# Kernel optimization log

Measured on AMD Instinct MI355X. Metric: run time of the kernel, lower is better.

The kernel has to match this reference:

```python
import jax, jax.numpy as jnp
import numpy as np

B, NC, NT = 16, 2048, 2048
IN_DIM, H_DIM, OUT_DIM = 128, 256, 256


def _mlp(x, w1, b1, w2, b2, w3, b3):
    # MLP(input_dim, [h, h], output_dim): Linear-ReLU-Linear-ReLU-Linear
    h = jax.nn.relu(x @ w1 + b1)
    h = jax.nn.relu(h @ w2 + b2)
    return h @ w3 + b3


def setup_inputs() -> dict:
    key = jax.random.key(0)
    ks = jax.random.split(key, 16)

    def lin(k, fan_in, fan_out):
        s = 1.0 / np.sqrt(fan_in)
        kw, kb = jax.random.split(k)
        w = jax.random.uniform(kw, (fan_in, fan_out), jnp.float32, -s, s)
        b = jax.random.uniform(kb, (fan_out,), jnp.float32, -s, s)
        return w, b

    qw1, qb1 = lin(ks[0], IN_DIM, H_DIM)
    qw2, qb2 = lin(ks[1], H_DIM, H_DIM)
    qw3, qb3 = lin(ks[2], H_DIM, OUT_DIM)
    kw1, kb1 = lin(ks[3], IN_DIM, H_DIM)
    kw2, kb2 = lin(ks[4], H_DIM, H_DIM)
    kw3, kb3 = lin(ks[5], H_DIM, OUT_DIM)

    return {
        "x_context": jax.random.normal(ks[6], (B, NC, IN_DIM), jnp.float32),
        "x_target": jax.random.normal(ks[7], (B, NT, IN_DIM), jnp.float32),
        "r_i": jax.random.normal(ks[8], (B, NC, OUT_DIM), jnp.float32),
        "qw1": qw1, "qb1": qb1, "qw2": qw2, "qb2": qb2, "qw3": qw3, "qb3": qb3,
        "kw1": kw1, "kb1": kb1, "kw2": kw2, "kb2": kb2, "kw3": kw3, "kb3": kb3,
    }


def reference(x_context, x_target, r_i,
              qw1, qb1, qw2, qb2, qw3, qb3,
              kw1, kb1, kw2, kb2, kw3, kb3):
    q = _mlp(x_target, qw1, qb1, qw2, qb2, qw3, qb3)   # [B, NT, D]
    k = _mlp(x_context, kw1, kb1, kw2, kb2, kw3, kb3)  # [B, NC, D]
    scale = jnp.sqrt(jnp.asarray(k.shape[-1], dtype=jnp.float32))
    w = jnp.einsum('btd,bcd->btc', q, k) / scale       # [B, NT, NC]
    # Faithful to torch.softmax(w, dim=1): normalize over the TARGET axis.
    w = jax.nn.softmax(w, axis=1)
    return jnp.einsum('btc,bcd->btd', w, r_i)          # [B, NT, OUT_DIM]
```

## Files before the change

kernel.cpp:

```cpp
#include <hip/hip_runtime.h>

#define BB 16
#define NT 2048
#define NC 2048
#define DIM 256
#define INDIM 128

typedef unsigned short u16;
typedef __bf16 bfx8 __attribute__((ext_vector_type(8)));
typedef __bf16 bfx8a __attribute__((ext_vector_type(8), aligned(8)));
typedef float f32x4 __attribute__((ext_vector_type(4)));

__device__ __forceinline__ u16 f2bf(float f) {
    union { float f; unsigned u; } v; v.f = f;
    return (u16)((v.u + 0x7FFFu + ((v.u >> 16) & 1u)) >> 16);
}

#define MFMA16(a, b, c) __builtin_amdgcn_mfma_f32_16x16x32_bf16((a), (b), (c), 0, 0, 0)


__global__ void cvt_w_kernel(const float* __restrict__ w, u16* __restrict__ wt, int K) {
    int idx = blockIdx.x * 256 + threadIdx.x;
    if (idx >= K * 256) return;
    int n = idx / K, k = idx - n * K;
    wt[idx] = f2bf(w[k * 256 + n]);
}

__global__ void cvt_rt_kernel(const float* __restrict__ r, u16* __restrict__ rt) {
    __shared__ u16 tile[32][33];
    int b = blockIdx.z;
    int c0 = blockIdx.x * 32, d0 = blockIdx.y * 32;
    int tx = threadIdx.x, ty = threadIdx.y;
    const float* rb = r + (size_t)b * NC * DIM;
#pragma unroll
    for (int i = 0; i < 4; i++) {
        int c = c0 + ty + i * 8;
        tile[ty + i * 8][tx] = f2bf(rb[(size_t)c * DIM + d0 + tx]);
    }
    __syncthreads();
    u16* rtb = rt + (size_t)b * DIM * NC;
#pragma unroll
    for (int i = 0; i < 4; i++) {
        int d = d0 + ty + i * 8;
        rtb[(size_t)d * NC + c0 + tx] = tile[tx][ty + i * 8];
    }
}


template <int K, bool RELU, bool CVTIN>
__global__ __launch_bounds__(256) void mlp_gemm(const void* __restrict__ Aq, const void* __restrict__ Ak,
                                                const u16* __restrict__ Wq, const u16* __restrict__ Wk,
                                                const float* __restrict__ bq, const float* __restrict__ bk,
                                                u16* __restrict__ Cq, u16* __restrict__ Ck) {
    constexpr int ROWB = K * 2;
    constexpr int NCH = K / 16;
    __shared__ __align__(16) u16 at[128 * K];

    int tid = threadIdx.x, lane = tid & 63, w = tid >> 6;
    int lr = lane & 15, lg = lane >> 4;
    int m0 = blockIdx.x * 128;
    bool isq = (blockIdx.y == 0);
    const u16* Wt = isq ? Wq : Wk;
    const float* bias = isq ? bq : bk;
    u16* C = isq ? Cq : Ck;

    if (CVTIN) {
        const float* A = (const float*)(isq ? Aq : Ak) + (size_t)m0 * K;
#pragma unroll
        for (int j = 0; j < NCH; j++) {
            int bo = tid * (NCH * 16) + j * 16;
            int row = bo >> 8;
            int ir = bo & (ROWB - 1);
            const float* src = A + (size_t)row * K + (ir >> 1);
            float4 f0 = *reinterpret_cast<const float4*>(src);
            float4 f1 = *reinterpret_cast<const float4*>(src + 4);
            union { u16 u[8]; uint4 v; } pk;
            {
                __bf16 h;
                h = (__bf16)f0.x; pk.u[0] = *(u16*)&h;
                h = (__bf16)f0.y; pk.u[1] = *(u16*)&h;
                h = (__bf16)f0.z; pk.u[2] = *(u16*)&h;
                h = (__bf16)f0.w; pk.u[3] = *(u16*)&h;
                h = (__bf16)f1.x; pk.u[4] = *(u16*)&h;
                h = (__bf16)f1.y; pk.u[5] = *(u16*)&h;
                h = (__bf16)f1.z; pk.u[6] = *(u16*)&h;
                h = (__bf16)f1.w; pk.u[7] = *(u16*)&h;
            }
            int dst = row * ROWB + (ir ^ ((row & 7) << 4));
            *reinterpret_cast<uint4*>((char*)at + dst) = pk.v;
        }
    } else {
        const char* A = (const char*)((const u16*)(isq ? Aq : Ak) + (size_t)m0 * K);
#pragma unroll
        for (int j = 0; j < NCH; j++) {
            int bo = j * 4096 + tid * 16;
            int row = bo >> 9;
            int ir = bo & (ROWB - 1);
            int sir = ir ^ ((row & 7) << 4);
            __builtin_amdgcn_global_load_lds(
                (const __attribute__((address_space(1))) void*)(A + (size_t)row * ROWB + sir),
                (__attribute__((address_space(3))) void*)((char*)at + bo),
                16, 0, 0);
        }
    }
    __syncthreads();

    int n0 = w * 64;
    f32x4 acc[8][4] = {};
#pragma unroll
    for (int ks = 0; ks < K / 32; ks++) {
        bfx8 b[4];
#pragma unroll
        for (int nt = 0; nt < 4; nt++)
            b[nt] = *reinterpret_cast<const bfx8*>(Wt + (size_t)(n0 + nt * 16 + lr) * K + ks * 32 + lg * 8);
#pragma unroll
        for (int mt = 0; mt < 8; mt++) {
            int row = mt * 16 + lr;
            int ir = (ks * 64 + lg * 16) ^ ((lr & 7) << 4);
            bfx8 a = *reinterpret_cast<const bfx8*>((const char*)at + row * ROWB + ir);
#pragma unroll
            for (int nt = 0; nt < 4; nt++)
                acc[mt][nt] = MFMA16(a, b[nt], acc[mt][nt]);
        }
    }

#pragma unroll
    for (int nt = 0; nt < 4; nt++) {
        int col = n0 + nt * 16 + lr;
        float bv = bias[col];
#pragma unroll
        for (int mt = 0; mt < 8; mt++) {
            int rowb = m0 + mt * 16 + lg * 4;
#pragma unroll
            for (int r = 0; r < 4; r++) {
                float v = acc[mt][nt][r] + bv;
                if (RELU) v = fmaxf(v, 0.0f);
                C[(size_t)(rowb + r) * 256 + col] = f2bf(v);
            }
        }
    }
}


__global__ __launch_bounds__(256) void stats_kernel(const u16* __restrict__ q,
                                                    const u16* __restrict__ k,
                                                    float2* __restrict__ gso) {
    int flat = blockIdx.x;
    int sw = (flat & 7) * 64 + (flat >> 3);
    int b = sw >> 5;
    int c0 = (sw & 31) * 64;
    int tid = threadIdx.x, lane = tid & 63, w = tid >> 6;
    int lr = lane & 15, lg = lane >> 4;
    const u16* qb = q + (size_t)b * NT * DIM;
    const u16* kb = k + (size_t)b * NC * DIM;
    const float scale = 1.0f / 16.0f;

    bfx8 kf[4][8];
#pragma unroll
    for (int j = 0; j < 4; j++)
#pragma unroll
        for (int ks = 0; ks < 8; ks++)
            kf[j][ks] = *reinterpret_cast<const bfx8*>(kb + (size_t)(c0 + j * 16 + lr) * DIM + ks * 32 + lg * 8);

    float m_run[4], l_run[4];
#pragma unroll
    for (int j = 0; j < 4; j++) { m_run[j] = -1e30f; l_run[j] = 0.0f; }

    for (int ts = 0; ts < NT / 64; ts++) {
        int t0 = ts * 64 + w * 16;
        f32x4 acc[4] = {};
#pragma unroll
        for (int ks = 0; ks < 8; ks++) {
            bfx8 a = *reinterpret_cast<const bfx8*>(qb + (size_t)(t0 + lr) * DIM + ks * 32 + lg * 8);
#pragma unroll
            for (int j = 0; j < 4; j++)
                acc[j] = MFMA16(a, kf[j][ks], acc[j]);
        }
#pragma unroll
        for (int j = 0; j < 4; j++) {
            float s0 = acc[j][0] * scale, s1 = acc[j][1] * scale;
            float s2 = acc[j][2] * scale, s3 = acc[j][3] * scale;
            float mx = fmaxf(fmaxf(s0, s1), fmaxf(s2, s3));
            mx = fmaxf(mx, __shfl_xor(mx, 16));
            mx = fmaxf(mx, __shfl_xor(mx, 32));
            float m_new = fmaxf(m_run[j], mx);
            float p = __expf(s0 - m_new) + __expf(s1 - m_new) + __expf(s2 - m_new) + __expf(s3 - m_new);
            p += __shfl_xor(p, 16);
            p += __shfl_xor(p, 32);
            l_run[j] = l_run[j] * __expf(m_run[j] - m_new) + p;
            m_run[j] = m_new;
        }
    }

    __shared__ float sm[4][64], sl[4][64];
    if (lg == 0) {
#pragma unroll
        for (int j = 0; j < 4; j++) {
            sm[w][j * 16 + lr] = m_run[j];
            sl[w][j * 16 + lr] = l_run[j];
        }
    }
    __syncthreads();
    if (tid < 64) {
        float mf = sm[0][tid];
#pragma unroll
        for (int ww = 1; ww < 4; ww++) mf = fmaxf(mf, sm[ww][tid]);
        float lf = 0.0f;
#pragma unroll
        for (int ww = 0; ww < 4; ww++) lf += sl[ww][tid] * __expf(sm[ww][tid] - mf);
        gso[(size_t)b * NC + c0 + tid] = make_float2(mf * 1.44269504f, 1.0f / lf);
    }
}


__global__ __launch_bounds__(256, 2) void attn_kernel(const u16* __restrict__ q,
                                                      const u16* __restrict__ k,
                                                      const u16* __restrict__ rt,
                                                      const float2* __restrict__ gsg_,
                                                      float* __restrict__ out) {
    int flat = blockIdx.x;
    int sw = (flat & 7) * 64 + (flat >> 3);
    int b = sw >> 5;
    int t0 = (sw & 31) * 64;
    int tid = threadIdx.x, lane = tid & 63, w = tid >> 6;
    int lr = lane & 15, lg = lane >> 4;
    const u16* qb = q + (size_t)b * NT * DIM;
    const u16* kb = k + (size_t)b * NC * DIM;
    const u16* rtb = rt + (size_t)b * DIM * NC;

    __shared__ float2 gs[NC];
    __shared__ __align__(16) u16 kt[2][32 * 256];
    __shared__ u16 pl[64][36];

    {
        const float2* gsg = gsg_ + (size_t)b * NC;
        for (int i = tid; i < NC; i += 256) gs[i] = gsg[i];
    }
    __syncthreads();

#define STAGE(nb, cc) do {                                                          \
    const u16* ksrc_ = kb + (size_t)(cc) * DIM;                                     \
    _Pragma("unroll")                                                               \
    for (int i_ = 0; i_ < 4; i_++) {                                                \
        int off_ = ((w * 4 + i_) << 10) + (lane << 4);                              \
        int row_ = off_ >> 9;                                                       \
        int ss_  = ((off_ >> 4) & 31) ^ (row_ & 7);                                 \
        const u16* g_ = ksrc_ + row_ * DIM + ss_ * 8;                               \
        __builtin_amdgcn_global_load_lds(                                           \
            (const __attribute__((address_space(1))) void*)g_,                      \
            (__attribute__((address_space(3))) void*)(&kt[nb][(w * 4 + i_) << 9]),  \
            16, 0, 0);                                                              \
    }                                                                               \
} while (0)

    STAGE(0, 0);
    __builtin_amdgcn_sched_barrier(0);
    bfx8 rb_c[4], rb_n[4];
#pragma unroll
    for (int nt = 0; nt < 4; nt++)
        rb_c[nt] = *reinterpret_cast<const bfx8*>(rtb + (size_t)(w * 64 + nt * 16 + lr) * NC + lg * 8);
    bfx8 aq[8];
#pragma unroll
    for (int ks = 0; ks < 8; ks++)
        aq[ks] = *reinterpret_cast<const bfx8*>(qb + (size_t)(t0 + w * 16 + lr) * DIM + ks * 32 + lg * 8);
    __builtin_amdgcn_sched_barrier(0);
    asm volatile("s_waitcnt vmcnt(12)");
    __builtin_amdgcn_s_barrier();
    __builtin_amdgcn_sched_barrier(0);

    const float A = 1.44269504f / 16.0f;
    const int key = lr & 7;
    f32x4 acc[4][4] = {};
    int cur = 0;

    for (int c0 = 0; c0 < NC; c0 += 32) {
        const bool last = (c0 + 32 >= NC);
        if (!last) STAGE(cur ^ 1, c0 + 32);
        __builtin_amdgcn_sched_barrier(0);
        if (!last) {
#pragma unroll
            for (int nt = 0; nt < 4; nt++)
                rb_n[nt] = *reinterpret_cast<const bfx8*>(rtb + (size_t)(w * 64 + nt * 16 + lr) * NC + (c0 + 32) + lg * 8);
        }

        f32x4 s[2] = {};
        {
            const char* kc = (const char*)&kt[cur][0];
#pragma unroll
            for (int ks = 0; ks < 8; ks++) {
                int slot = (ks << 2) | lg;
                bfx8 k0 = *reinterpret_cast<const bfx8*>(kc + (lr << 9) + (((slot ^ key)) << 4));
                bfx8 k1 = *reinterpret_cast<const bfx8*>(kc + ((16 + lr) << 9) + (((slot ^ key)) << 4));
                s[0] = MFMA16(aq[ks], k0, s[0]);
                s[1] = MFMA16(aq[ks], k1, s[1]);
            }
        }
#pragma unroll
        for (int j = 0; j < 2; j++) {
            float2 g = gs[c0 + j * 16 + lr];
#pragma unroll
            for (int r = 0; r < 4; r++) {
                float p = exp2f(fmaf(s[j][r], A, -g.x)) * g.y;
                __bf16 h = (__bf16)p;
                pl[w * 16 + lg * 4 + r][j * 16 + lr] = *(u16*)&h;
            }
        }
        __builtin_amdgcn_sched_barrier(0);
        asm volatile("s_waitcnt lgkmcnt(0)");
        __builtin_amdgcn_s_barrier();
        __builtin_amdgcn_sched_barrier(0);

#pragma unroll
        for (int mt = 0; mt < 4; mt++) {
            bfx8a pa = *reinterpret_cast<const bfx8a*>((const char*)pl + (mt * 16 + lr) * 72 + lg * 16);
#pragma unroll
            for (int nt = 0; nt < 4; nt++)
                acc[mt][nt] = MFMA16((bfx8)pa, rb_c[nt], acc[mt][nt]);
        }

        __builtin_amdgcn_sched_barrier(0);
        asm volatile("s_waitcnt vmcnt(4) lgkmcnt(0)");
        __builtin_amdgcn_s_barrier();
        __builtin_amdgcn_sched_barrier(0);

#pragma unroll
        for (int nt = 0; nt < 4; nt++) rb_c[nt] = rb_n[nt];
        cur ^= 1;
    }
#undef STAGE

    float* ob = out + (size_t)b * NT * DIM;
#pragma unroll
    for (int nt = 0; nt < 4; nt++) {
        int col = w * 64 + nt * 16 + lr;
#pragma unroll
        for (int mt = 0; mt < 4; mt++) {
            int rowb = t0 + mt * 16 + lg * 4;
#pragma unroll
            for (int r = 0; r < 4; r++)
                ob[(size_t)(rowb + r) * DIM + col] = acc[mt][nt][r];
        }
    }
}


extern "C" void kernel_launch(void* const* d_in, const int* in_sizes, int n_in,
                              void* d_out, int out_size, void* d_ws, size_t ws_size,
                              hipStream_t stream) {
    const float* xc  = (const float*)d_in[0];
    const float* xt  = (const float*)d_in[1];
    const float* ri  = (const float*)d_in[2];
    const float* qw1 = (const float*)d_in[3];  const float* qb1 = (const float*)d_in[4];
    const float* qw2 = (const float*)d_in[5];  const float* qb2 = (const float*)d_in[6];
    const float* qw3 = (const float*)d_in[7];  const float* qb3 = (const float*)d_in[8];
    const float* kw1 = (const float*)d_in[9];  const float* kb1 = (const float*)d_in[10];
    const float* kw2 = (const float*)d_in[11]; const float* kb2 = (const float*)d_in[12];
    const float* kw3 = (const float*)d_in[13]; const float* kb3 = (const float*)d_in[14];

    if (ws_size < ((size_t)66 << 20)) return;

    char* ws = (char*)d_ws;
    u16* h1q = (u16*)(ws);
    u16* h1k = (u16*)(ws + ((size_t)16 << 20));
    u16* q   = h1q;
    u16* kk  = h1k;
    u16* h2q = (u16*)(ws + ((size_t)32 << 20));
    u16* h2k = (u16*)(ws + ((size_t)48 << 20));
    u16* rt  = h2q;
    float2* gsb = (float2*)(ws + ((size_t)64 << 20));
    u16* wbuf = (u16*)(ws + ((size_t)64 << 20) + (512 << 10));
    u16* qw1t = wbuf;
    u16* qw2t = qw1t + 32768;
    u16* qw3t = qw2t + 65536;
    u16* kw1t = qw3t + 65536;
    u16* kw2t = kw1t + 32768;
    u16* kw3t = kw2t + 65536;

    cvt_w_kernel<<<dim3(128), 256, 0, stream>>>(qw1, qw1t, 128);
    cvt_w_kernel<<<dim3(256), 256, 0, stream>>>(qw2, qw2t, 256);
    cvt_w_kernel<<<dim3(256), 256, 0, stream>>>(qw3, qw3t, 256);
    cvt_w_kernel<<<dim3(128), 256, 0, stream>>>(kw1, kw1t, 128);
    cvt_w_kernel<<<dim3(256), 256, 0, stream>>>(kw2, kw2t, 256);
    cvt_w_kernel<<<dim3(256), 256, 0, stream>>>(kw3, kw3t, 256);

    mlp_gemm<128, true,  true ><<<dim3(256, 2), 256, 0, stream>>>(xt, xc, qw1t, kw1t, qb1, kb1, h1q, h1k);
    mlp_gemm<256, true,  false><<<dim3(256, 2), 256, 0, stream>>>(h1q, h1k, qw2t, kw2t, qb2, kb2, h2q, h2k);
    mlp_gemm<256, false, false><<<dim3(256, 2), 256, 0, stream>>>(h2q, h2k, qw3t, kw3t, qb3, kb3, q, kk);

    cvt_rt_kernel<<<dim3(64, 8, BB), dim3(32, 8), 0, stream>>>(ri, rt);

    stats_kernel<<<dim3(512), 256, 0, stream>>>(q, kk, gsb);

    attn_kernel<<<dim3(512), 256, 0, stream>>>(q, kk, rt, gsb, (float*)d_out);
}
```

Baseline: 286.4 us.

## Split attention block across 8 waves, defer stats shuffles, merge weight casts

The attention kernel now runs 512 threads per block. Each wave computes one 16x16 score tile and a 32x64 slice of the output instead of 64x64, and softmax stats are streamed from global memory rather than staged in shared memory. The stats kernel drops the per-step cross-lane max/sum shuffles in favour of per-lane online stats that are merged once at the end, using exp2 with a prescaled constant. The six weight-conversion launches are fused into one. Together these aim for more waves in flight to hide latency, fewer shuffles, and less launch overhead. The trade-off is more barrier participants per block and register pressure under the new launch bounds.

```diff
diff --git a/kernel.cpp b/kernel.cpp
--- a/kernel.cpp
+++ b/kernel.cpp
@@ -19,11 +19,22 @@
 #define MFMA16(a, b, c) __builtin_amdgcn_mfma_f32_16x16x32_bf16((a), (b), (c), 0, 0, 0)
 
 
-__global__ void cvt_w_kernel(const float* __restrict__ w, u16* __restrict__ wt, int K) {
-    int idx = blockIdx.x * 256 + threadIdx.x;
-    if (idx >= K * 256) return;
+__global__ void cvt_w_all(const float* __restrict__ w0, const float* __restrict__ w1,
+                          const float* __restrict__ w2, const float* __restrict__ w3,
+                          const float* __restrict__ w4, const float* __restrict__ w5,
+                          u16* __restrict__ o0, u16* __restrict__ o1, u16* __restrict__ o2,
+                          u16* __restrict__ o3, u16* __restrict__ o4, u16* __restrict__ o5) {
+    int bx = blockIdx.x;
+    const float* src; u16* dst; int K, base;
+    if (bx < 128)       { src = w0; dst = o0; K = 128; base = 0; }
+    else if (bx < 384)  { src = w1; dst = o1; K = 256; base = 128; }
+    else if (bx < 640)  { src = w2; dst = o2; K = 256; base = 384; }
+    else if (bx < 768)  { src = w3; dst = o3; K = 128; base = 640; }
+    else if (bx < 1024) { src = w4; dst = o4; K = 256; base = 768; }
+    else                { src = w5; dst = o5; K = 256; base = 1024; }
+    int idx = (bx - base) * 256 + threadIdx.x;
     int n = idx / K, k = idx - n * K;
-    wt[idx] = f2bf(w[k * 256 + n]);
+    dst[idx] = f2bf(src[k * 256 + n]);
 }
 
 __global__ void cvt_rt_kernel(const float* __restrict__ r, u16* __restrict__ rt) {
@@ -153,7 +164,7 @@
     int lr = lane & 15, lg = lane >> 4;
     const u16* qb = q + (size_t)b * NT * DIM;
     const u16* kb = k + (size_t)b * NC * DIM;
-    const float scale = 1.0f / 16.0f;
+    const float A2 = 1.44269504f / 16.0f;
 
     bfx8 kf[4][8];
 #pragma unroll
@@ -178,18 +189,29 @@
         }
 #pragma unroll
         for (int j = 0; j < 4; j++) {
-            float s0 = acc[j][0] * scale, s1 = acc[j][1] * scale;
-            float s2 = acc[j][2] * scale, s3 = acc[j][3] * scale;
-            float mx = fmaxf(fmaxf(s0, s1), fmaxf(s2, s3));
-            mx = fmaxf(mx, __shfl_xor(mx, 16));
-            mx = fmaxf(mx, __shfl_xor(mx, 32));
-            float m_new = fmaxf(m_run[j], mx);
-            float p = __expf(s0 - m_new) + __expf(s1 - m_new) + __expf(s2 - m_new) + __expf(s3 - m_new);
-            p += __shfl_xor(p, 16);
-            p += __shfl_xor(p, 32);
-            l_run[j] = l_run[j] * __expf(m_run[j] - m_new) + p;
-            m_run[j] = m_new;
-        }
+            f32x4 a = acc[j];
+            float mx = fmaxf(fmaxf(a[0], a[1]), fmaxf(a[2], a[3]));
+            float mn = fmaxf(m_run[j], mx);
+            float t = mn * A2;
+            float sum = exp2f(fmaf(a[0], A2, -t)) + exp2f(fmaf(a[1], A2, -t)) +
+                        exp2f(fmaf(a[2], A2, -t)) + exp2f(fmaf(a[3], A2, -t));
+            l_run[j] = l_run[j] * exp2f(fmaf(m_run[j], A2, -t)) + sum;
+            m_run[j] = mn;
+        }
+    }
+
+#pragma unroll
+    for (int j = 0; j < 4; j++) {
+        float m = m_run[j], l = l_run[j];
+#pragma unroll
+        for (int d = 16; d < 64; d <<= 1) {
+            float mo = __shfl_xor(m, d);
+            float lo = __shfl_xor(l, d);
+            float mn = fmaxf(m, mo);
+            l = l * exp2f((m - mn) * A2) + lo * exp2f((mo - mn) * A2);
+            m = mn;
+        }
+        m_run[j] = m; l_run[j] = l;
     }
 
     __shared__ float sm[4][64], sl[4][64];
@@ -207,13 +229,13 @@
         for (int ww = 1; ww < 4; ww++) mf = fmaxf(mf, sm[ww][tid]);
         float lf = 0.0f;
 #pragma unroll
-        for (int ww = 0; ww < 4; ww++) lf += sl[ww][tid] * __expf(sm[ww][tid] - mf);
-        gso[(size_t)b * NC + c0 + tid] = make_float2(mf * 1.44269504f, 1.0f / lf);
-    }
-}
-
-
-__global__ __launch_bounds__(256, 2) void attn_kernel(const u16* __restrict__ q,
+        for (int ww = 0; ww < 4; ww++) lf += sl[ww][tid] * exp2f((sm[ww][tid] - mf) * A2);
+        gso[(size_t)b * NC + c0 + tid] = make_float2(mf * A2, 1.0f / lf);
+    }
+}
+
+
+__global__ __launch_bounds__(512, 4) void attn_kernel(const u16* __restrict__ q,
                                                       const u16* __restrict__ k,
                                                       const u16* __restrict__ rt,
                                                       const float2* __restrict__ gsg_,
@@ -224,53 +246,51 @@
     int t0 = (sw & 31) * 64;
     int tid = threadIdx.x, lane = tid & 63, w = tid >> 6;
     int lr = lane & 15, lg = lane >> 4;
+    int sr = w & 3, sc = w >> 2;
+    int pr = w & 1, pc = w >> 1;
     const u16* qb = q + (size_t)b * NT * DIM;
     const u16* kb = k + (size_t)b * NC * DIM;
     const u16* rtb = rt + (size_t)b * DIM * NC;
-
-    __shared__ float2 gs[NC];
+    const float2* gsg = gsg_ + (size_t)b * NC;
+
     __shared__ __align__(16) u16 kt[2][32 * 256];
     __shared__ u16 pl[64][36];
-
-    {
-        const float2* gsg = gsg_ + (size_t)b * NC;
-        for (int i = tid; i < NC; i += 256) gs[i] = gsg[i];
-    }
-    __syncthreads();
 
 #define STAGE(nb, cc) do {                                                          \
     const u16* ksrc_ = kb + (size_t)(cc) * DIM;                                     \
     _Pragma("unroll")                                                               \
-    for (int i_ = 0; i_ < 4; i_++) {                                                \
-        int off_ = ((w * 4 + i_) << 10) + (lane << 4);                              \
+    for (int i_ = 0; i_ < 2; i_++) {                                                \
+        int off_ = ((w * 2 + i_) << 10) + (lane << 4);                              \
         int row_ = off_ >> 9;                                                       \
         int ss_  = ((off_ >> 4) & 31) ^ (row_ & 7);                                 \
         const u16* g_ = ksrc_ + row_ * DIM + ss_ * 8;                               \
         __builtin_amdgcn_global_load_lds(                                           \
             (const __attribute__((address_space(1))) void*)g_,                      \
-            (__attribute__((address_space(3))) void*)(&kt[nb][(w * 4 + i_) << 9]),  \
+            (__attribute__((address_space(3))) void*)(&kt[nb][(w * 2 + i_) << 9]),  \
             16, 0, 0);                                                              \
     }                                                                               \
 } while (0)
 
     STAGE(0, 0);
     __builtin_amdgcn_sched_barrier(0);
+    float2 gs_c, gs_n;
+    gs_c = gsg[sc * 16 + lr];
     bfx8 rb_c[4], rb_n[4];
 #pragma unroll
     for (int nt = 0; nt < 4; nt++)
-        rb_c[nt] = *reinterpret_cast<const bfx8*>(rtb + (size_t)(w * 64 + nt * 16 + lr) * NC + lg * 8);
+        rb_c[nt] = *reinterpret_cast<const bfx8*>(rtb + (size_t)(pc * 64 + nt * 16 + lr) * NC + lg * 8);
     bfx8 aq[8];
 #pragma unroll
     for (int ks = 0; ks < 8; ks++)
-        aq[ks] = *reinterpret_cast<const bfx8*>(qb + (size_t)(t0 + w * 16 + lr) * DIM + ks * 32 + lg * 8);
+        aq[ks] = *reinterpret_cast<const bfx8*>(qb + (size_t)(t0 + sr * 16 + lr) * DIM + ks * 32 + lg * 8);
     __builtin_amdgcn_sched_barrier(0);
-    asm volatile("s_waitcnt vmcnt(12)");
+    asm volatile("s_waitcnt vmcnt(13)");
     __builtin_amdgcn_s_barrier();
     __builtin_amdgcn_sched_barrier(0);
 
     const float A = 1.44269504f / 16.0f;
     const int key = lr & 7;
-    f32x4 acc[4][4] = {};
+    f32x4 acc[2][4] = {};
     int cur = 0;
 
     for (int c0 = 0; c0 < NC; c0 += 32) {
@@ -278,32 +298,27 @@
         if (!last) STAGE(cur ^ 1, c0 + 32);
         __builtin_amdgcn_sched_barrier(0);
         if (!last) {
+            gs_n = gsg[c0 + 32 + sc * 16 + lr];
 #pragma unroll
             for (int nt = 0; nt < 4; nt++)
-                rb_n[nt] = *reinterpret_cast<const bfx8*>(rtb + (size_t)(w * 64 + nt * 16 + lr) * NC + (c0 + 32) + lg * 8);
-        }
-
-        f32x4 s[2] = {};
+                rb_n[nt] = *reinterpret_cast<const bfx8*>(rtb + (size_t)(pc * 64 + nt * 16 + lr) * NC + (c0 + 32) + lg * 8);
+        }
+
+        f32x4 s = {};
         {
             const char* kc = (const char*)&kt[cur][0];
 #pragma unroll
             for (int ks = 0; ks < 8; ks++) {
                 int slot = (ks << 2) | lg;
-                bfx8 k0 = *reinterpret_cast<const bfx8*>(kc + (lr << 9) + (((slot ^ key)) << 4));
-                bfx8 k1 = *reinterpret_cast<const bfx8*>(kc + ((16 + lr) << 9) + (((slot ^ key)) << 4));
-                s[0] = MFMA16(aq[ks], k0, s[0]);
-                s[1] = MFMA16(aq[ks], k1, s[1]);
+                bfx8 kf = *reinterpret_cast<const bfx8*>(kc + ((sc * 16 + lr) << 9) + ((slot ^ key) << 4));
+                s = MFMA16(aq[ks], kf, s);
             }
         }
 #pragma unroll
-        for (int j = 0; j < 2; j++) {
-            float2 g = gs[c0 + j * 16 + lr];
-#pragma unroll
-            for (int r = 0; r < 4; r++) {
-                float p = exp2f(fmaf(s[j][r], A, -g.x)) * g.y;
-                __bf16 h = (__bf16)p;
-                pl[w * 16 + lg * 4 + r][j * 16 + lr] = *(u16*)&h;
-            }
+        for (int r = 0; r < 4; r++) {
+            float p = exp2f(fmaf(s[r], A, -gs_c.x)) * gs_c.y;
+            __bf16 h = (__bf16)p;
+            pl[sr * 16 + lg * 4 + r][sc * 16 + lr] = *(u16*)&h;
         }
         __builtin_amdgcn_sched_barrier(0);
         asm volatile("s_waitcnt lgkmcnt(0)");
@@ -311,31 +326,32 @@
         __builtin_amdgcn_sched_barrier(0);
 
 #pragma unroll
-        for (int mt = 0; mt < 4; mt++) {
-            bfx8a pa = *reinterpret_cast<const bfx8a*>((const char*)pl + (mt * 16 + lr) * 72 + lg * 16);
+        for (int mt = 0; mt < 2; mt++) {
+            bfx8a pa = *reinterpret_cast<const bfx8a*>((const char*)pl + (pr * 32 + mt * 16 + lr) * 72 + lg * 16);
 #pragma unroll
             for (int nt = 0; nt < 4; nt++)
                 acc[mt][nt] = MFMA16((bfx8)pa, rb_c[nt], acc[mt][nt]);
         }
 
         __builtin_amdgcn_sched_barrier(0);
-        asm volatile("s_waitcnt vmcnt(4) lgkmcnt(0)");
+        asm volatile("s_waitcnt vmcnt(5) lgkmcnt(0)");
         __builtin_amdgcn_s_barrier();
         __builtin_amdgcn_sched_barrier(0);
 
 #pragma unroll
         for (int nt = 0; nt < 4; nt++) rb_c[nt] = rb_n[nt];
+        gs_c = gs_n;
         cur ^= 1;
     }
 #undef STAGE
 
     float* ob = out + (size_t)b * NT * DIM;
 #pragma unroll
-    for (int nt = 0; nt < 4; nt++) {
-        int col = w * 64 + nt * 16 + lr;
-#pragma unroll
-        for (int mt = 0; mt < 4; mt++) {
-            int rowb = t0 + mt * 16 + lg * 4;
+    for (int mt = 0; mt < 2; mt++) {
+#pragma unroll
+        for (int nt = 0; nt < 4; nt++) {
+            int col = pc * 64 + nt * 16 + lr;
+            int rowb = t0 + pr * 32 + mt * 16 + lg * 4;
 #pragma unroll
             for (int r = 0; r < 4; r++)
                 ob[(size_t)(rowb + r) * DIM + col] = acc[mt][nt][r];
@@ -376,12 +392,8 @@
     u16* kw2t = kw1t + 32768;
     u16* kw3t = kw2t + 65536;
 
-    cvt_w_kernel<<<dim3(128), 256, 0, stream>>>(qw1, qw1t, 128);
-    cvt_w_kernel<<<dim3(256), 256, 0, stream>>>(qw2, qw2t, 256);
-    cvt_w_kernel<<<dim3(256), 256, 0, stream>>>(qw3, qw3t, 256);
-    cvt_w_kernel<<<dim3(128), 256, 0, stream>>>(kw1, kw1t, 128);
-    cvt_w_kernel<<<dim3(256), 256, 0, stream>>>(kw2, kw2t, 256);
-    cvt_w_kernel<<<dim3(256), 256, 0, stream>>>(kw3, kw3t, 256);
+    cvt_w_all<<<dim3(1280), 256, 0, stream>>>(qw1, qw2, qw3, kw1, kw2, kw3,
+                                              qw1t, qw2t, qw3t, kw1t, kw2t, kw3t);
 
     mlp_gemm<128, true,  true ><<<dim3(256, 2), 256, 0, stream>>>(xt, xc, qw1t, kw1t, qb1, kb1, h1q, h1k);
     mlp_gemm<256, true,  false><<<dim3(256, 2), 256, 0, stream>>>(h1q, h1k, qw2t, kw2t, qb2, kb2, h2q, h2k);
@@ -391,5 +403,5 @@
 
     stats_kernel<<<dim3(512), 256, 0, stream>>>(q, kk, gsb);
 
-    attn_kernel<<<dim3(512), 256, 0, stream>>>(q, kk, rt, gsb, (float*)d_out);
-}
+    attn_kernel<<<dim3(512), 512, 0, stream>>>(q, kk, rt, gsb, (float*)d_out);
+}
```

Measured after the change: 413.2 us. 44.3% more time.
